# Kernel tuning notes

Hardware: AMD Instinct MI355X
Metric: run time of the kernel (lower is better)

The kernel has to match this reference:

```python
import jax, jax.numpy as jnp
import numpy as np

N, H, E, T, ED, AB = 50000, 64, 800000, 800000, 64, 16


def setup_inputs() -> dict:
    key = jax.random.key(0)
    ks = jax.random.split(key, 26)

    def nrm(k, shape, scale=1.0):
        return jax.random.normal(k, shape, dtype=jnp.float32) * scale

    d = {}
    d["s"] = nrm(ks[0], (N, H))
    d["v"] = nrm(ks[1], (N, H, 3))
    d["edge_index"] = jax.random.randint(ks[2], (2, E), 0, N, dtype=jnp.int32)
    d["edge_rbf"] = jax.random.uniform(ks[3], (E, ED), dtype=jnp.float32)
    raw_dir = jax.random.normal(ks[4], (E, 3), dtype=jnp.float32)
    d["edge_dir"] = raw_dir / jnp.linalg.norm(raw_dir, axis=-1, keepdims=True)
    d["triplet_kj"] = jax.random.randint(ks[5], (T,), 0, E, dtype=jnp.int32)
    d["triplet_ji"] = jax.random.randint(ks[6], (T,), 0, E, dtype=jnp.int32)
    d["angle_feat"] = jax.random.uniform(ks[7], (T, AB), dtype=jnp.float32)

    def lin(kw, kb, fan_in, fan_out):
        sc = 1.0 / np.sqrt(fan_in)
        return nrm(kw, (fan_in, fan_out), sc), nrm(kb, (fan_out,), sc)

    d["W_t1"], d["b_t1"] = lin(ks[8], ks[9], 2 * ED + AB, H)
    d["W_t2"], d["b_t2"] = lin(ks[10], ks[11], H, H)
    d["W_m1"], d["b_m1"] = lin(ks[12], ks[13], 2 * H + ED + H, H)
    d["W_m2"], d["b_m2"] = lin(ks[14], ks[15], H, 2 * H)
    d["W_u1"], d["b_u1"] = lin(ks[16], ks[17], 3 * H, H)
    d["W_u2"], d["b_u2"] = lin(ks[18], ks[19], H, H)
    d["W_g1"], d["b_g1"] = lin(ks[20], ks[21], 3 * H, H)
    d["W_g2"], d["b_g2"] = lin(ks[22], ks[23], H, H)
    d["ln_g"] = jnp.ones((H,), jnp.float32)
    d["ln_b"] = jnp.zeros((H,), jnp.float32)
    return d


def _mlp(x, W1, b1, W2, b2):
    return jax.nn.silu(x @ W1 + b1) @ W2 + b2


def reference(s, v, edge_index, edge_rbf, edge_dir, triplet_kj, triplet_ji,
              angle_feat, W_t1, b_t1, W_t2, b_t2, W_m1, b_m1, W_m2, b_m2,
              W_u1, b_u1, W_u2, b_u2, W_g1, b_g1, W_g2, b_g2, ln_g, ln_b):
    n_nodes, hid = s.shape
    n_edges = edge_rbf.shape[0]

    # 3-body triplet messages: gather two edge rbf rows + angle feature
    t_in = jnp.concatenate([edge_rbf[triplet_kj], edge_rbf[triplet_ji], angle_feat], axis=-1)
    t_msg = _mlp(t_in, W_t1, b_t1, W_t2, b_t2)                 # [T, H]
    angle_agg = jax.ops.segment_sum(t_msg, triplet_ji, num_segments=n_edges)  # [E, H]

    src, dst = edge_index[0], edge_index[1]
    msg_in = jnp.concatenate([s[src], s[dst], edge_rbf, angle_agg], axis=-1)  # [E, 4H]
    msg = _mlp(msg_in, W_m1, b_m1, W_m2, b_m2)                 # [E, 2H]
    m_s, m_v_coeff = jnp.split(msg, 2, axis=-1)

    agg_s = jax.ops.segment_sum(m_s, dst, num_segments=n_nodes)  # [N, H]
    m_v = m_v_coeff[:, :, None] * edge_dir[:, None, :]          # [E, H, 3]
    agg_v = jax.ops.segment_sum(m_v.reshape(n_edges, hid * 3), dst,
                                num_segments=n_nodes).reshape(n_nodes, hid, 3)

    v_norm = jnp.linalg.norm(v, axis=-1)                        # [N, H]
    ctx = jnp.concatenate([s, agg_s, v_norm], axis=-1)          # [N, 3H]
    s_new = s + _mlp(ctx, W_u1, b_u1, W_u2, b_u2)
    gate = jax.nn.sigmoid(_mlp(ctx, W_g1, b_g1, W_g2, b_g2))
    v_new = v + gate[..., None] * agg_v

    mu = s_new.mean(axis=-1, keepdims=True)
    var = s_new.var(axis=-1, keepdims=True)
    s_ln = (s_new - mu) / jnp.sqrt(var + 1e-5) * ln_g + ln_b
    s_out = jax.nn.silu(s_ln)
    return (s_out, v_new)
```

## Files before the change

kernel.cpp:

```cpp
#include <hip/hip_runtime.h>
#include <cstdint>
#include <cstddef>

#define NN 50000
#define NE 800000
#define NT 800000

typedef unsigned short u16;
typedef unsigned int u32;
typedef __attribute__((ext_vector_type(8))) short short8;
typedef __attribute__((ext_vector_type(4))) float f32x4;

__device__ __forceinline__ float silu_f(float x) { return x / (1.f + __expf(-x)); }
__device__ __forceinline__ float sigm_f(float x) { return 1.f / (1.f + __expf(-x)); }
__device__ __forceinline__ u16 f2b(float x) {
  u32 u = __float_as_uint(x);
  u32 r = u + 0x7fffu + ((u >> 16) & 1u);
  return (u16)(r >> 16);
}
__device__ __forceinline__ float b2f(u16 h) { return __uint_as_float(((u32)h) << 16); }

template <int RW>
__device__ __forceinline__ int lx(int r, int c) {
  return r * RW + ((((c >> 3) ^ (r & 7)) << 3) | (c & 7));
}

__global__ __launch_bounds__(256) void kcvt(const float* __restrict__ in,
                                            u16* __restrict__ out, int n4) {
  int i = blockIdx.x * 256 + threadIdx.x;
  if (i >= n4) return;
  float4 v = ((const float4*)in)[i];
  uint2 p;
  p.x = (u32)f2b(v.x) | ((u32)f2b(v.y) << 16);
  p.y = (u32)f2b(v.z) | ((u32)f2b(v.w) << 16);
  ((uint2*)out)[i] = p;
}

__global__ __launch_bounds__(256) void khist(const int* __restrict__ keys, int n,
                                             int* __restrict__ cnt) {
  int i = blockIdx.x * 256 + threadIdx.x;
  if (i < n) atomicAdd(&cnt[keys[i]], 1);
}

__global__ __launch_bounds__(256) void kscan1(const int* __restrict__ in, int n,
                                              int* __restrict__ out, int* __restrict__ bsum) {
  __shared__ int sh[256];
  int tid = threadIdx.x;
  size_t base = (size_t)blockIdx.x * 1024;
  int v[4];
  int acc = 0;
#pragma unroll
  for (int q = 0; q < 4; ++q) {
    size_t i = base + (size_t)tid * 4 + q;
    int x = (i < (size_t)n) ? in[i] : 0;
    v[q] = acc;
    acc += x;
  }
  sh[tid] = acc;
  __syncthreads();
  for (int off = 1; off < 256; off <<= 1) {
    int y = (tid >= off) ? sh[tid - off] : 0;
    __syncthreads();
    sh[tid] += y;
    __syncthreads();
  }
  int excl = (tid == 0) ? 0 : sh[tid - 1];
  if (tid == 255) bsum[blockIdx.x] = sh[255];
#pragma unroll
  for (int q = 0; q < 4; ++q) {
    size_t i = base + (size_t)tid * 4 + q;
    if (i < (size_t)n) out[i] = excl + v[q];
  }
}

__global__ __launch_bounds__(1024) void kscan2(int* __restrict__ bsum, int nb) {
  __shared__ int sh[1024];
  int tid = threadIdx.x;
  sh[tid] = (tid < nb) ? bsum[tid] : 0;
  __syncthreads();
  for (int off = 1; off < 1024; off <<= 1) {
    int y = (tid >= off) ? sh[tid - off] : 0;
    __syncthreads();
    sh[tid] += y;
    __syncthreads();
  }
  if (tid < nb) bsum[tid] = (tid == 0) ? 0 : sh[tid - 1];
}

__global__ __launch_bounds__(256) void kscan3(int* __restrict__ out, const int* __restrict__ bsum,
                                              int n, int total) {
  int i = blockIdx.x * 256 + threadIdx.x;
  if (i < n) out[i] += bsum[i >> 10];
  else if (i == n) out[n] = total;
}

__global__ __launch_bounds__(256) void kscatter_inv(const int* __restrict__ keys,
                                                    const int* __restrict__ off, int n,
                                                    int* __restrict__ cnt, int* __restrict__ inv) {
  int i = blockIdx.x * 256 + threadIdx.x;
  if (i < n) {
    int k = keys[i];
    int slot = off[k] + (atomicSub(&cnt[k], 1) - 1);
    inv[i] = slot;
  }
}

__global__ __launch_bounds__(256) void kscatter_inv_dir(const int* __restrict__ keys,
                                                        const int* __restrict__ off, int n,
                                                        int* __restrict__ cnt, int* __restrict__ inv,
                                                        const float* __restrict__ dir,
                                                        float* __restrict__ dir_s) {
  int i = blockIdx.x * 256 + threadIdx.x;
  if (i < n) {
    int k = keys[i];
    int slot = off[k] + (atomicSub(&cnt[k], 1) - 1);
    inv[i] = slot;
    dir_s[(size_t)slot * 3 + 0] = dir[(size_t)i * 3 + 0];
    dir_s[(size_t)slot * 3 + 1] = dir[(size_t)i * 3 + 1];
    dir_s[(size_t)slot * 3 + 2] = dir[(size_t)i * 3 + 2];
  }
}

__global__ __launch_bounds__(256) void kprepw(const float* __restrict__ W, int K, int Kp, int N,
                                              u16* __restrict__ out) {
  int tid = blockIdx.x * 256 + threadIdx.x;
  int total = (Kp / 32) * (N / 16) * 64;
  if (tid >= total) return;
  int l = tid & 63;
  int f = tid >> 6;
  int nt = f % (N / 16);
  int kt = f / (N / 16);
  int k0 = kt * 32 + (l >> 4) * 8;
  int n = nt * 16 + (l & 15);
  u16 vals[8];
#pragma unroll
  for (int j = 0; j < 8; ++j) {
    int kk = k0 + j;
    vals[j] = (kk < K) ? f2b(W[(size_t)kk * N + n]) : (u16)0;
  }
  uint4* dst = (uint4*)(out + (size_t)f * 512 + l * 8);
  uint4 p;
  p.x = (u32)vals[0] | ((u32)vals[1] << 16);
  p.y = (u32)vals[2] | ((u32)vals[3] << 16);
  p.z = (u32)vals[4] | ((u32)vals[5] << 16);
  p.w = (u32)vals[6] | ((u32)vals[7] << 16);
  *dst = p;
}

__global__ __launch_bounds__(256) void ktrip_mfma(
    const int* __restrict__ tkj, const int* __restrict__ tji,
    const u16* __restrict__ erbf_bf, const u16* __restrict__ afeat_bf,
    const int* __restrict__ tslot,
    const u16* __restrict__ Wp1, const float* __restrict__ b1,
    const u16* __restrict__ Wp2, const float* __restrict__ b2,
    u16* __restrict__ tmsg_s) {
  __shared__ u16 Xs[64 * 192];
  __shared__ u16 Hs[64 * 64];
  const int tid = threadIdx.x;
  const int l = tid & 63;
  const int w = tid >> 6;
  const int t0 = blockIdx.x * 64;

#pragma unroll
  for (int it = 0; it < 4; ++it) {
    int idx = it * 256 + tid;
    int sel = idx >> 9, r = (idx >> 3) & 63, ch = idx & 7;
    int t = t0 + r;
    int node = sel ? tji[t] : tkj[t];
    uint4 vv = *(const uint4*)&erbf_bf[(size_t)node * 64 + ch * 8];
    *(uint4*)&Xs[lx<192>(r, sel * 64 + ch * 8)] = vv;
  }
  {
    int r = tid >> 2, c = (tid & 3) * 4;
    uint2 p2 = *(const uint2*)&afeat_bf[(size_t)(t0 + r) * 16 + c];
    *(uint2*)&Xs[lx<192>(r, 128 + c)] = p2;
  }
#pragma unroll
  for (int i = 0; i < 2; ++i) {
    int idx = i * 256 + tid;
    int r = idx >> 3, c = 144 + (idx & 7) * 2;
    *(u32*)&Xs[lx<192>(r, c)] = 0;
  }
  __syncthreads();

  f32x4 acc1[4];
  {
    float bias = b1[w * 16 + (l & 15)];
#pragma unroll
    for (int mt = 0; mt < 4; ++mt) acc1[mt] = (f32x4){bias, bias, bias, bias};
    for (int ks = 0; ks < 5; ++ks) {
      short8 bf = *(const short8*)(Wp1 + ((size_t)(ks * 4 + w) * 64 + l) * 8);
#pragma unroll
      for (int mt = 0; mt < 4; ++mt) {
        short8 af = *(const short8*)&Xs[lx<192>(mt * 16 + (l & 15), ks * 32 + ((l >> 4) << 3))];
        acc1[mt] = __builtin_amdgcn_mfma_f32_16x16x32_bf16(af, bf, acc1[mt], 0, 0, 0);
      }
    }
  }
#pragma unroll
  for (int mt = 0; mt < 4; ++mt)
#pragma unroll
    for (int q = 0; q < 4; ++q) {
      int r = mt * 16 + (l >> 4) * 4 + q;
      Hs[lx<64>(r, w * 16 + (l & 15))] = f2b(silu_f(acc1[mt][q]));
    }
  __syncthreads();

  f32x4 acc2[4];
  {
    float bias = b2[w * 16 + (l & 15)];
#pragma unroll
    for (int mt = 0; mt < 4; ++mt) acc2[mt] = (f32x4){bias, bias, bias, bias};
    for (int ks = 0; ks < 2; ++ks) {
      short8 bf = *(const short8*)(Wp2 + ((size_t)(ks * 4 + w) * 64 + l) * 8);
#pragma unroll
      for (int mt = 0; mt < 4; ++mt) {
        short8 af = *(const short8*)&Hs[lx<64>(mt * 16 + (l & 15), ks * 32 + ((l >> 4) << 3))];
        acc2[mt] = __builtin_amdgcn_mfma_f32_16x16x32_bf16(af, bf, acc2[mt], 0, 0, 0);
      }
    }
  }
  __syncthreads();
#pragma unroll
  for (int mt = 0; mt < 4; ++mt)
#pragma unroll
    for (int q = 0; q < 4; ++q) {
      int r = mt * 16 + (l >> 4) * 4 + q;
      Xs[lx<64>(r, w * 16 + (l & 15))] = f2b(acc2[mt][q]);
    }
  __syncthreads();
  for (int i = 0; i < 2; ++i) {
    int idx = i * 256 + tid;
    int r = idx >> 3, c0 = (idx & 7) << 3;
    int slot = tslot[t0 + r];
    uint4 val = *(const uint4*)&Xs[lx<64>(r, c0)];
    *(uint4*)(tmsg_s + (size_t)slot * 64 + c0) = val;
  }
}

__global__ __launch_bounds__(256) void kmsg_mfma(
    const int* __restrict__ eidx, const u16* __restrict__ s_bf,
    const u16* __restrict__ erbf_bf,
    const int* __restrict__ toff, const u16* __restrict__ tmsg_s,
    const int* __restrict__ eslot,
    const u16* __restrict__ Wp1, const float* __restrict__ b1,
    const u16* __restrict__ Wp2, const float* __restrict__ b2,
    u16* __restrict__ msg_s) {
  __shared__ u16 Xs[64 * 256];
  __shared__ u16 Hs[64 * 64];
  const int tid = threadIdx.x;
  const int l = tid & 63;
  const int w = tid >> 6;
  const int e0 = blockIdx.x * 64;

#pragma unroll
  for (int i = 0; i < 2; ++i) {
    int idx = i * 256 + tid;
    int r = idx >> 3, c0 = (idx & 7) << 3;
    uint4 vv = *(const uint4*)&erbf_bf[(size_t)(e0 + r) * 64 + c0];
    *(uint4*)&Xs[lx<256>(r, 128 + c0)] = vv;
  }
#pragma unroll
  for (int it = 0; it < 4; ++it) {
    int idx = it * 256 + tid;
    int sel = idx >> 9, r = (idx >> 3) & 63, ch = idx & 7;
    int node = eidx[sel * NE + e0 + r];
    uint4 vv = *(const uint4*)&s_bf[(size_t)node * 64 + ch * 8];
    *(uint4*)&Xs[lx<256>(r, sel * 64 + ch * 8)] = vv;
  }
#pragma unroll
  for (int it = 0; it < 2; ++it) {
    int idx = it * 256 + tid;
    int r = idx >> 3, ch = idx & 7;
    int e = e0 + r;
    int r0 = toff[e], r1 = toff[e + 1];
    float a[8];
#pragma unroll
    for (int j = 0; j < 8; ++j) a[j] = 0.f;
    for (int ri = r0; ri < r1; ++ri) {
      uint4 pk = *(const uint4*)&tmsg_s[(size_t)ri * 64 + ch * 8];
      a[0] += b2f((u16)(pk.x & 0xffff)); a[1] += b2f((u16)(pk.x >> 16));
      a[2] += b2f((u16)(pk.y & 0xffff)); a[3] += b2f((u16)(pk.y >> 16));
      a[4] += b2f((u16)(pk.z & 0xffff)); a[5] += b2f((u16)(pk.z >> 16));
      a[6] += b2f((u16)(pk.w & 0xffff)); a[7] += b2f((u16)(pk.w >> 16));
    }
    uint4 p;
    p.x = (u32)f2b(a[0]) | ((u32)f2b(a[1]) << 16);
    p.y = (u32)f2b(a[2]) | ((u32)f2b(a[3]) << 16);
    p.z = (u32)f2b(a[4]) | ((u32)f2b(a[5]) << 16);
    p.w = (u32)f2b(a[6]) | ((u32)f2b(a[7]) << 16);
    *(uint4*)&Xs[lx<256>(r, 192 + ch * 8)] = p;
  }
  __syncthreads();

  f32x4 acc1[4];
  {
    float bias = b1[w * 16 + (l & 15)];
#pragma unroll
    for (int mt = 0; mt < 4; ++mt) acc1[mt] = (f32x4){bias, bias, bias, bias};
    for (int ks = 0; ks < 8; ++ks) {
      short8 bf = *(const short8*)(Wp1 + ((size_t)(ks * 4 + w) * 64 + l) * 8);
#pragma unroll
      for (int mt = 0; mt < 4; ++mt) {
        short8 af = *(const short8*)&Xs[lx<256>(mt * 16 + (l & 15), ks * 32 + ((l >> 4) << 3))];
        acc1[mt] = __builtin_amdgcn_mfma_f32_16x16x32_bf16(af, bf, acc1[mt], 0, 0, 0);
      }
    }
  }
#pragma unroll
  for (int mt = 0; mt < 4; ++mt)
#pragma unroll
    for (int q = 0; q < 4; ++q) {
      int r = mt * 16 + (l >> 4) * 4 + q;
      Hs[lx<64>(r, w * 16 + (l & 15))] = f2b(silu_f(acc1[mt][q]));
    }
  __syncthreads();

  f32x4 acc2[2][4];
#pragma unroll
  for (int pp = 0; pp < 2; ++pp) {
    int nt = w * 2 + pp;
    float bias = b2[nt * 16 + (l & 15)];
#pragma unroll
    for (int mt = 0; mt < 4; ++mt) acc2[pp][mt] = (f32x4){bias, bias, bias, bias};
    for (int ks = 0; ks < 2; ++ks) {
      short8 bf = *(const short8*)(Wp2 + ((size_t)(ks * 8 + nt) * 64 + l) * 8);
#pragma unroll
      for (int mt = 0; mt < 4; ++mt) {
        short8 af = *(const short8*)&Hs[lx<64>(mt * 16 + (l & 15), ks * 32 + ((l >> 4) << 3))];
        acc2[pp][mt] = __builtin_amdgcn_mfma_f32_16x16x32_bf16(af, bf, acc2[pp][mt], 0, 0, 0);
      }
    }
  }
  __syncthreads();
#pragma unroll
  for (int pp = 0; pp < 2; ++pp)
#pragma unroll
    for (int mt = 0; mt < 4; ++mt)
#pragma unroll
      for (int q = 0; q < 4; ++q) {
        int r = mt * 16 + (l >> 4) * 4 + q;
        Xs[lx<128>(r, (w * 2 + pp) * 16 + (l & 15))] = f2b(acc2[pp][mt][q]);
      }
  __syncthreads();
  for (int i = 0; i < 4; ++i) {
    int idx = i * 256 + tid;
    int r = idx >> 4, c0 = (idx & 15) << 3;
    int slot = eslot[e0 + r];
    uint4 val = *(const uint4*)&Xs[lx<128>(r, c0)];
    *(uint4*)(msg_s + (size_t)slot * 128 + c0) = val;
  }
}

__global__ __launch_bounds__(256) void kagg(
    const int* __restrict__ noff, const u16* __restrict__ msg_s,
    const float* __restrict__ dir_s,
    u16* __restrict__ aggs_bf, float* __restrict__ aggv) {
  const int lane = threadIdx.x & 63;
  const int wv = threadIdx.x >> 6;
  const int n = blockIdx.x * 4 + wv;
  if (n >= NN) return;
  const int r0 = noff[n], r1 = noff[n + 1];
  const int half = lane >> 5, m = lane & 31;
  float a0 = 0.f, a1 = 0.f;
  float v00 = 0.f, v01 = 0.f, v02 = 0.f, v10 = 0.f, v11 = 0.f, v12 = 0.f;
  for (int r = r0; r < r1; ++r) {
    u32 pk = *(const u32*)&msg_s[(size_t)r * 128 + lane * 2];
    float x0 = b2f((u16)(pk & 0xffff));
    float x1 = b2f((u16)(pk >> 16));
    if (half == 0) {
      a0 += x0; a1 += x1;
    } else {
      float dx = dir_s[(size_t)r * 3 + 0];
      float dy = dir_s[(size_t)r * 3 + 1];
      float dz = dir_s[(size_t)r * 3 + 2];
      v00 += x0 * dx; v01 += x0 * dy; v02 += x0 * dz;
      v10 += x1 * dx; v11 += x1 * dy; v12 += x1 * dz;
    }
  }
  if (half == 0) {
    *(u32*)&aggs_bf[(size_t)n * 64 + m * 2] = (u32)f2b(a0) | ((u32)f2b(a1) << 16);
  } else {
    float* av = aggv + (size_t)n * 192 + (size_t)(m * 2) * 3;
    av[0] = v00; av[1] = v01; av[2] = v02;
    av[3] = v10; av[4] = v11; av[5] = v12;
  }
}

__global__ __launch_bounds__(256) void knode_mfma(
    const u16* __restrict__ s_bf, const float* __restrict__ v,
    const u16* __restrict__ aggs_bf, const float* __restrict__ aggv,
    const u16* __restrict__ WpU1, const float* __restrict__ bU1,
    const u16* __restrict__ WpU2, const float* __restrict__ bU2,
    const u16* __restrict__ WpG1, const float* __restrict__ bG1,
    const u16* __restrict__ WpG2, const float* __restrict__ bG2,
    const float* __restrict__ lng, const float* __restrict__ lnb,
    float* __restrict__ outs, float* __restrict__ outv) {
  __shared__ __align__(16) char smem[64 * 192 * 2 + 2 * 64 * 64 * 2];
  u16* Xs = (u16*)smem;
  u16* Hu = (u16*)(smem + 64 * 192 * 2);
  u16* Hg = Hu + 64 * 64;
  float* Fs = (float*)smem;

  const int tid = threadIdx.x;
  const int l = tid & 63;
  const int w = tid >> 6;
  const int n0 = blockIdx.x * 64;

  for (int i = 0; i < 2; ++i) {
    int idx = i * 256 + tid;
    int r = idx >> 3, c0 = (idx & 7) << 3;
    int nr = n0 + r; if (nr >= NN) nr = NN - 1;
    uint4 a = *(const uint4*)&s_bf[(size_t)nr * 64 + c0];
    *(uint4*)&Xs[lx<192>(r, c0)] = a;
    uint4 b = *(const uint4*)&aggs_bf[(size_t)nr * 64 + c0];
    *(uint4*)&Xs[lx<192>(r, 64 + c0)] = b;
  }
  for (int it = 0; it < 16; ++it) {
    int idx = it * 256 + tid;
    int r = idx >> 6, c = idx & 63;
    int nr = n0 + r; if (nr >= NN) nr = NN - 1;
    const float* vp = v + (size_t)nr * 192 + c * 3;
    float x = vp[0], y = vp[1], z = vp[2];
    Xs[lx<192>(r, 128 + c)] = f2b(sqrtf(x * x + y * y + z * z));
  }
  __syncthreads();

  f32x4 au[4], ag[4];
  {
    float biu = bU1[w * 16 + (l & 15)], big = bG1[w * 16 + (l & 15)];
#pragma unroll
    for (int mt = 0; mt < 4; ++mt) {
      au[mt] = (f32x4){biu, biu, biu, biu};
      ag[mt] = (f32x4){big, big, big, big};
    }
    for (int ks = 0; ks < 6; ++ks) {
      short8 bu = *(const short8*)(WpU1 + ((size_t)(ks * 4 + w) * 64 + l) * 8);
      short8 bg = *(const short8*)(WpG1 + ((size_t)(ks * 4 + w) * 64 + l) * 8);
#pragma unroll
      for (int mt = 0; mt < 4; ++mt) {
        short8 af = *(const short8*)&Xs[lx<192>(mt * 16 + (l & 15), ks * 32 + ((l >> 4) << 3))];
        au[mt] = __builtin_amdgcn_mfma_f32_16x16x32_bf16(af, bu, au[mt], 0, 0, 0);
        ag[mt] = __builtin_amdgcn_mfma_f32_16x16x32_bf16(af, bg, ag[mt], 0, 0, 0);
      }
    }
  }
#pragma unroll
  for (int mt = 0; mt < 4; ++mt)
#pragma unroll
    for (int q = 0; q < 4; ++q) {
      int r = mt * 16 + (l >> 4) * 4 + q;
      Hu[lx<64>(r, w * 16 + (l & 15))] = f2b(silu_f(au[mt][q]));
      Hg[lx<64>(r, w * 16 + (l & 15))] = f2b(silu_f(ag[mt][q]));
    }
  __syncthreads();

  f32x4 ou[4], og[4];
  {
    float biu = bU2[w * 16 + (l & 15)], big = bG2[w * 16 + (l & 15)];
#pragma unroll
    for (int mt = 0; mt < 4; ++mt) {
      ou[mt] = (f32x4){biu, biu, biu, biu};
      og[mt] = (f32x4){big, big, big, big};
    }
    for (int ks = 0; ks < 2; ++ks) {
      short8 bu = *(const short8*)(WpU2 + ((size_t)(ks * 4 + w) * 64 + l) * 8);
      short8 bg = *(const short8*)(WpG2 + ((size_t)(ks * 4 + w) * 64 + l) * 8);
#pragma unroll
      for (int mt = 0; mt < 4; ++mt) {
        short8 afu = *(const short8*)&Hu[lx<64>(mt * 16 + (l & 15), ks * 32 + ((l >> 4) << 3))];
        ou[mt] = __builtin_amdgcn_mfma_f32_16x16x32_bf16(afu, bu, ou[mt], 0, 0, 0);
        short8 afg = *(const short8*)&Hg[lx<64>(mt * 16 + (l & 15), ks * 32 + ((l >> 4) << 3))];
        og[mt] = __builtin_amdgcn_mfma_f32_16x16x32_bf16(afg, bg, og[mt], 0, 0, 0);
      }
    }
  }
#pragma unroll
  for (int mt = 0; mt < 4; ++mt)
#pragma unroll
    for (int q = 0; q < 4; ++q) {
      int r = mt * 16 + (l >> 4) * 4 + q;
      ou[mt][q] += b2f(Xs[lx<192>(r, w * 16 + (l & 15))]);
    }
  __syncthreads();

#pragma unroll
  for (int mt = 0; mt < 4; ++mt)
#pragma unroll
    for (int q = 0; q < 4; ++q) {
      int r = mt * 16 + (l >> 4) * 4 + q;
      Fs[r * 68 + w * 16 + (l & 15)] = ou[mt][q];
    }
  __syncthreads();
  {
    int r = tid >> 2, c0 = (tid & 3) * 16;
    float xv[16];
#pragma unroll
    for (int j4 = 0; j4 < 4; ++j4) {
      float4 t = *(const float4*)&Fs[r * 68 + c0 + j4 * 4];
      xv[j4 * 4 + 0] = t.x; xv[j4 * 4 + 1] = t.y;
      xv[j4 * 4 + 2] = t.z; xv[j4 * 4 + 3] = t.w;
    }
    float sm = 0.f, sq = 0.f;
#pragma unroll
    for (int j = 0; j < 16; ++j) { sm += xv[j]; sq += xv[j] * xv[j]; }
    sm += __shfl_xor(sm, 1); sq += __shfl_xor(sq, 1);
    sm += __shfl_xor(sm, 2); sq += __shfl_xor(sq, 2);
    float mu = sm * (1.f / 64.f);
    float var = sq * (1.f / 64.f) - mu * mu;
    float rstd = rsqrtf(var + 1e-5f);
    if (n0 + r < NN) {
      float* op = outs + (size_t)(n0 + r) * 64 + c0;
#pragma unroll
      for (int j4 = 0; j4 < 4; ++j4) {
        float4 o;
        float y0 = (xv[j4 * 4 + 0] - mu) * rstd * lng[c0 + j4 * 4 + 0] + lnb[c0 + j4 * 4 + 0];
        float y1 = (xv[j4 * 4 + 1] - mu) * rstd * lng[c0 + j4 * 4 + 1] + lnb[c0 + j4 * 4 + 1];
        float y2 = (xv[j4 * 4 + 2] - mu) * rstd * lng[c0 + j4 * 4 + 2] + lnb[c0 + j4 * 4 + 2];
        float y3 = (xv[j4 * 4 + 3] - mu) * rstd * lng[c0 + j4 * 4 + 3] + lnb[c0 + j4 * 4 + 3];
        o.x = silu_f(y0); o.y = silu_f(y1); o.z = silu_f(y2); o.w = silu_f(y3);
        *(float4*)(op + j4 * 4) = o;
      }
    }
  }
  __syncthreads();

#pragma unroll
  for (int mt = 0; mt < 4; ++mt)
#pragma unroll
    for (int q = 0; q < 4; ++q) {
      int r = mt * 16 + (l >> 4) * 4 + q;
      Fs[r * 68 + w * 16 + (l & 15)] = og[mt][q];
    }
  __syncthreads();
  {
    int r = tid >> 2, c0 = (tid & 3) * 16;
    int nr = n0 + r;
    if (nr < NN) {
      float gate[16];
#pragma unroll
      for (int j = 0; j < 16; ++j) gate[j] = sigm_f(Fs[r * 68 + c0 + j]);
      const float4* vp = (const float4*)(v + (size_t)nr * 192 + c0 * 3);
      const float4* ap = (const float4*)(aggv + (size_t)nr * 192 + c0 * 3);
      float4* op = (float4*)(outv + (size_t)nr * 192 + c0 * 3);
#pragma unroll
      for (int j4 = 0; j4 < 12; ++j4) {
        float4 vv = vp[j4], av = ap[j4], o;
        o.x = vv.x + gate[(j4 * 4 + 0) / 3] * av.x;
        o.y = vv.y + gate[(j4 * 4 + 1) / 3] * av.y;
        o.z = vv.z + gate[(j4 * 4 + 2) / 3] * av.z;
        o.w = vv.w + gate[(j4 * 4 + 3) / 3] * av.w;
        op[j4] = o;
      }
    }
  }
}

extern "C" void kernel_launch(void* const* d_in, const int* in_sizes, int n_in,
                              void* d_out, int out_size, void* d_ws, size_t ws_size,
                              hipStream_t stream) {
  const float* s     = (const float*)d_in[0];
  const float* v     = (const float*)d_in[1];
  const int*   eidx  = (const int*)d_in[2];
  const float* erbf  = (const float*)d_in[3];
  const float* edir  = (const float*)d_in[4];
  const int*   tkj   = (const int*)d_in[5];
  const int*   tji   = (const int*)d_in[6];
  const float* afeat = (const float*)d_in[7];
  const float* W_t1  = (const float*)d_in[8];
  const float* b_t1  = (const float*)d_in[9];
  const float* W_t2  = (const float*)d_in[10];
  const float* b_t2  = (const float*)d_in[11];
  const float* W_m1  = (const float*)d_in[12];
  const float* b_m1  = (const float*)d_in[13];
  const float* W_m2  = (const float*)d_in[14];
  const float* b_m2  = (const float*)d_in[15];
  const float* W_u1  = (const float*)d_in[16];
  const float* b_u1  = (const float*)d_in[17];
  const float* W_u2  = (const float*)d_in[18];
  const float* b_u2  = (const float*)d_in[19];
  const float* W_g1  = (const float*)d_in[20];
  const float* b_g1  = (const float*)d_in[21];
  const float* W_g2  = (const float*)d_in[22];
  const float* b_g2  = (const float*)d_in[23];
  const float* ln_g  = (const float*)d_in[24];
  const float* ln_b  = (const float*)d_in[25];

  char* w = (char*)d_ws;
  auto alloc = [&](size_t bytes) -> char* {
    char* p = w;
    w += (bytes + 255) & ~(size_t)255;
    return p;
  };
  int* toff  = (int*)alloc((size_t)(NE + 1) * 4);
  int* noff  = (int*)alloc((size_t)(NN + 1) * 4);
  int* tcnt  = (int*)alloc((size_t)NE * 4);
  int* ncnt  = (int*)alloc((size_t)NN * 4);
  int* tslot = (int*)alloc((size_t)NT * 4);
  int* eslot = (int*)alloc((size_t)NE * 4);
  int* bsum  = (int*)alloc(1024 * 4);
  float* dir_s = (float*)alloc((size_t)NE * 3 * 4);
  u16* msg_s  = (u16*)alloc((size_t)NE * 128 * 2);
  u16* tmsg_s = (u16*)alloc((size_t)NT * 64 * 2);
  u16* erbf_bf = (u16*)alloc((size_t)NE * 64 * 2);
  u16* s_bf    = (u16*)alloc((size_t)NN * 64 * 2);
  u16* Wp_t1 = (u16*)alloc((size_t)5 * 4 * 512 * 2);
  u16* Wp_t2 = (u16*)alloc((size_t)2 * 4 * 512 * 2);
  u16* Wp_m1 = (u16*)alloc((size_t)8 * 4 * 512 * 2);
  u16* Wp_m2 = (u16*)alloc((size_t)2 * 8 * 512 * 2);
  u16* Wp_u1 = (u16*)alloc((size_t)6 * 4 * 512 * 2);
  u16* Wp_u2 = (u16*)alloc((size_t)2 * 4 * 512 * 2);
  u16* Wp_g1 = (u16*)alloc((size_t)6 * 4 * 512 * 2);
  u16* Wp_g2 = (u16*)alloc((size_t)2 * 4 * 512 * 2);
  u16* afeat_bf = msg_s;
  float* aggv = (float*)tmsg_s;
  u16* aggs_bf = tmsg_s + (size_t)NN * 384;

  hipMemsetAsync(tcnt, 0, (size_t)NE * 4, stream);
  hipMemsetAsync(ncnt, 0, (size_t)NN * 4, stream);

  kcvt<<<(NE * 16 + 255) / 256, 256, 0, stream>>>(erbf, erbf_bf, NE * 16);
  kcvt<<<(NN * 16 + 255) / 256, 256, 0, stream>>>(s, s_bf, NN * 16);
  kcvt<<<(NT * 4 + 255) / 256, 256, 0, stream>>>(afeat, afeat_bf, NT * 4);

  khist<<<(NT + 255) / 256, 256, 0, stream>>>(tji, NT, tcnt);
  khist<<<(NE + 255) / 256, 256, 0, stream>>>(eidx + NE, NE, ncnt);

  kscan1<<<(NE + 1023) / 1024, 256, 0, stream>>>(tcnt, NE, toff, bsum);
  kscan2<<<1, 1024, 0, stream>>>(bsum, (NE + 1023) / 1024);
  kscan3<<<(NE + 1 + 255) / 256, 256, 0, stream>>>(toff, bsum, NE, NT);
  kscatter_inv<<<(NT + 255) / 256, 256, 0, stream>>>(tji, toff, NT, tcnt, tslot);

  kscan1<<<(NN + 1023) / 1024, 256, 0, stream>>>(ncnt, NN, noff, bsum);
  kscan2<<<1, 1024, 0, stream>>>(bsum, (NN + 1023) / 1024);
  kscan3<<<(NN + 1 + 255) / 256, 256, 0, stream>>>(noff, bsum, NN, NE);
  kscatter_inv_dir<<<(NE + 255) / 256, 256, 0, stream>>>(eidx + NE, noff, NE, ncnt, eslot,
                                                         edir, dir_s);

  kprepw<<<5, 256, 0, stream>>>(W_t1, 144, 160, 64, Wp_t1);
  kprepw<<<2, 256, 0, stream>>>(W_t2, 64, 64, 64, Wp_t2);
  kprepw<<<8, 256, 0, stream>>>(W_m1, 256, 256, 64, Wp_m1);
  kprepw<<<4, 256, 0, stream>>>(W_m2, 64, 64, 128, Wp_m2);
  kprepw<<<6, 256, 0, stream>>>(W_u1, 192, 192, 64, Wp_u1);
  kprepw<<<2, 256, 0, stream>>>(W_u2, 64, 64, 64, Wp_u2);
  kprepw<<<6, 256, 0, stream>>>(W_g1, 192, 192, 64, Wp_g1);
  kprepw<<<2, 256, 0, stream>>>(W_g2, 64, 64, 64, Wp_g2);

  ktrip_mfma<<<NT / 64, 256, 0, stream>>>(tkj, tji, erbf_bf, afeat_bf, tslot,
                                          Wp_t1, b_t1, Wp_t2, b_t2, tmsg_s);
  kmsg_mfma<<<NE / 64, 256, 0, stream>>>(eidx, s_bf, erbf_bf, toff, tmsg_s, eslot,
                                         Wp_m1, b_m1, Wp_m2, b_m2, msg_s);
  kagg<<<(NN + 3) / 4, 256, 0, stream>>>(noff, msg_s, dir_s, aggs_bf, aggv);

  float* out_s = (float*)d_out;
  float* out_v = out_s + (size_t)NN * 64;
  knode_mfma<<<(NN + 63) / 64, 256, 0, stream>>>(s_bf, v, aggs_bf, aggv,
                                                 Wp_u1, b_u1, Wp_u2, b_u2,
                                                 Wp_g1, b_g1, Wp_g2, b_g2,
                                                 ln_g, ln_b, out_s, out_v);
}
```

Baseline: 726.7 us.

## Process triplets in sorted order, fuse afeat conversion into scatter, vectorize aggregation

The triplet kernel now iterates over triplets in their sorted-by-ji order, using an inverse permutation (tids), so its output rows are written contiguously instead of scattered through tslot. The angle-feature bf16 conversion is folded into the scatter kernel, which writes afeat already permuted into sorted order, removing one conversion launch. The node aggregation kernel is rewritten so each lane loads 16-byte chunks and four edge rows are processed per iteration, followed by a cross-lane shuffle reduction and vectorized stores. Trade-offs: the triplet kernel now does an extra indirect lookup per row, and the scatter kernel writes afeat at random slots.

```diff
diff --git a/kernel.cpp b/kernel.cpp
--- a/kernel.cpp
+++ b/kernel.cpp
@@ -94,14 +94,25 @@
   else if (i == n) out[n] = total;
 }
 
-__global__ __launch_bounds__(256) void kscatter_inv(const int* __restrict__ keys,
-                                                    const int* __restrict__ off, int n,
-                                                    int* __restrict__ cnt, int* __restrict__ inv) {
+__global__ __launch_bounds__(256) void kscatter_inv_afeat(
+    const int* __restrict__ keys, const int* __restrict__ off, int n,
+    int* __restrict__ cnt, int* __restrict__ tids,
+    const float* __restrict__ afeat, u16* __restrict__ afeat_s) {
   int i = blockIdx.x * 256 + threadIdx.x;
   if (i < n) {
     int k = keys[i];
     int slot = off[k] + (atomicSub(&cnt[k], 1) - 1);
-    inv[i] = slot;
+    tids[slot] = i;
+    const float4* src = (const float4*)(afeat + (size_t)i * 16);
+    uint2* dst = (uint2*)(afeat_s + (size_t)slot * 16);
+#pragma unroll
+    for (int q = 0; q < 4; ++q) {
+      float4 v = src[q];
+      uint2 p;
+      p.x = (u32)f2b(v.x) | ((u32)f2b(v.y) << 16);
+      p.y = (u32)f2b(v.z) | ((u32)f2b(v.w) << 16);
+      dst[q] = p;
+    }
   }
 }
 
@@ -149,8 +160,8 @@
 
 __global__ __launch_bounds__(256) void ktrip_mfma(
     const int* __restrict__ tkj, const int* __restrict__ tji,
-    const u16* __restrict__ erbf_bf, const u16* __restrict__ afeat_bf,
-    const int* __restrict__ tslot,
+    const u16* __restrict__ erbf_bf, const u16* __restrict__ afeat_s,
+    const int* __restrict__ tids,
     const u16* __restrict__ Wp1, const float* __restrict__ b1,
     const u16* __restrict__ Wp2, const float* __restrict__ b2,
     u16* __restrict__ tmsg_s) {
@@ -159,20 +170,20 @@
   const int tid = threadIdx.x;
   const int l = tid & 63;
   const int w = tid >> 6;
-  const int t0 = blockIdx.x * 64;
+  const int st0 = blockIdx.x * 64;
 
 #pragma unroll
   for (int it = 0; it < 4; ++it) {
     int idx = it * 256 + tid;
     int sel = idx >> 9, r = (idx >> 3) & 63, ch = idx & 7;
-    int t = t0 + r;
+    int t = tids[st0 + r];
     int node = sel ? tji[t] : tkj[t];
     uint4 vv = *(const uint4*)&erbf_bf[(size_t)node * 64 + ch * 8];
     *(uint4*)&Xs[lx<192>(r, sel * 64 + ch * 8)] = vv;
   }
   {
     int r = tid >> 2, c = (tid & 3) * 4;
-    uint2 p2 = *(const uint2*)&afeat_bf[(size_t)(t0 + r) * 16 + c];
+    uint2 p2 = *(const uint2*)&afeat_s[(size_t)(st0 + r) * 16 + c];
     *(uint2*)&Xs[lx<192>(r, 128 + c)] = p2;
   }
 #pragma unroll
@@ -232,9 +243,8 @@
   for (int i = 0; i < 2; ++i) {
     int idx = i * 256 + tid;
     int r = idx >> 3, c0 = (idx & 7) << 3;
-    int slot = tslot[t0 + r];
     uint4 val = *(const uint4*)&Xs[lx<64>(r, c0)];
-    *(uint4*)(tmsg_s + (size_t)slot * 64 + c0) = val;
+    *(uint4*)(tmsg_s + (size_t)(st0 + r) * 64 + c0) = val;
   }
 }
 
@@ -361,29 +371,64 @@
   const int n = blockIdx.x * 4 + wv;
   if (n >= NN) return;
   const int r0 = noff[n], r1 = noff[n + 1];
-  const int half = lane >> 5, m = lane & 31;
-  float a0 = 0.f, a1 = 0.f;
-  float v00 = 0.f, v01 = 0.f, v02 = 0.f, v10 = 0.f, v11 = 0.f, v12 = 0.f;
-  for (int r = r0; r < r1; ++r) {
-    u32 pk = *(const u32*)&msg_s[(size_t)r * 128 + lane * 2];
-    float x0 = b2f((u16)(pk & 0xffff));
-    float x1 = b2f((u16)(pk >> 16));
-    if (half == 0) {
-      a0 += x0; a1 += x1;
+  const int lrow = lane >> 4, lcol = lane & 15;
+  const bool is_ms = (lcol < 8);
+
+  float a[8];
+  float v0[8], v1[8], v2[8];
+#pragma unroll
+  for (int j = 0; j < 8; ++j) { a[j] = 0.f; v0[j] = 0.f; v1[j] = 0.f; v2[j] = 0.f; }
+
+  for (int r4 = r0; r4 < r1; r4 += 4) {
+    int r = r4 + lrow;
+    if (r < r1) {
+      uint4 pk = *(const uint4*)&msg_s[(size_t)r * 128 + lcol * 8];
+      float x[8];
+      x[0] = b2f((u16)(pk.x & 0xffff)); x[1] = b2f((u16)(pk.x >> 16));
+      x[2] = b2f((u16)(pk.y & 0xffff)); x[3] = b2f((u16)(pk.y >> 16));
+      x[4] = b2f((u16)(pk.z & 0xffff)); x[5] = b2f((u16)(pk.z >> 16));
+      x[6] = b2f((u16)(pk.w & 0xffff)); x[7] = b2f((u16)(pk.w >> 16));
+      if (is_ms) {
+#pragma unroll
+        for (int j = 0; j < 8; ++j) a[j] += x[j];
+      } else {
+        float dx = dir_s[(size_t)r * 3 + 0];
+        float dy = dir_s[(size_t)r * 3 + 1];
+        float dz = dir_s[(size_t)r * 3 + 2];
+#pragma unroll
+        for (int j = 0; j < 8; ++j) {
+          v0[j] += x[j] * dx; v1[j] += x[j] * dy; v2[j] += x[j] * dz;
+        }
+      }
+    }
+  }
+#pragma unroll
+  for (int j = 0; j < 8; ++j) {
+    a[j] += __shfl_xor(a[j], 16);  a[j] += __shfl_xor(a[j], 32);
+    v0[j] += __shfl_xor(v0[j], 16); v0[j] += __shfl_xor(v0[j], 32);
+    v1[j] += __shfl_xor(v1[j], 16); v1[j] += __shfl_xor(v1[j], 32);
+    v2[j] += __shfl_xor(v2[j], 16); v2[j] += __shfl_xor(v2[j], 32);
+  }
+  if (lrow == 0) {
+    if (is_ms) {
+      uint4 p;
+      p.x = (u32)f2b(a[0]) | ((u32)f2b(a[1]) << 16);
+      p.y = (u32)f2b(a[2]) | ((u32)f2b(a[3]) << 16);
+      p.z = (u32)f2b(a[4]) | ((u32)f2b(a[5]) << 16);
+      p.w = (u32)f2b(a[6]) | ((u32)f2b(a[7]) << 16);
+      *(uint4*)&aggs_bf[(size_t)n * 64 + lcol * 8] = p;
     } else {
-      float dx = dir_s[(size_t)r * 3 + 0];
-      float dy = dir_s[(size_t)r * 3 + 1];
-      float dz = dir_s[(size_t)r * 3 + 2];
-      v00 += x0 * dx; v01 += x0 * dy; v02 += x0 * dz;
-      v10 += x1 * dx; v11 += x1 * dy; v12 += x1 * dz;
-    }
-  }
-  if (half == 0) {
-    *(u32*)&aggs_bf[(size_t)n * 64 + m * 2] = (u32)f2b(a0) | ((u32)f2b(a1) << 16);
-  } else {
-    float* av = aggv + (size_t)n * 192 + (size_t)(m * 2) * 3;
-    av[0] = v00; av[1] = v01; av[2] = v02;
-    av[3] = v10; av[4] = v11; av[5] = v12;
+      int c0 = (lcol - 8) * 8;
+      float* av = aggv + (size_t)n * 192 + (size_t)c0 * 3;
+      float4 o0 = {v0[0], v1[0], v2[0], v0[1]};
+      float4 o1 = {v1[1], v2[1], v0[2], v1[2]};
+      float4 o2 = {v2[2], v0[3], v1[3], v2[3]};
+      float4 o3 = {v0[4], v1[4], v2[4], v0[5]};
+      float4 o4 = {v1[5], v2[5], v0[6], v1[6]};
+      float4 o5 = {v2[6], v0[7], v1[7], v2[7]};
+      float4* av4 = (float4*)av;
+      av4[0] = o0; av4[1] = o1; av4[2] = o2; av4[3] = o3; av4[4] = o4; av4[5] = o5;
+    }
   }
 }
 
@@ -596,7 +641,7 @@
   int* noff  = (int*)alloc((size_t)(NN + 1) * 4);
   int* tcnt  = (int*)alloc((size_t)NE * 4);
   int* ncnt  = (int*)alloc((size_t)NN * 4);
-  int* tslot = (int*)alloc((size_t)NT * 4);
+  int* tids  = (int*)alloc((size_t)NT * 4);
   int* eslot = (int*)alloc((size_t)NE * 4);
   int* bsum  = (int*)alloc(1024 * 4);
   float* dir_s = (float*)alloc((size_t)NE * 3 * 4);
@@ -612,7 +657,7 @@
   u16* Wp_u2 = (u16*)alloc((size_t)2 * 4 * 512 * 2);
   u16* Wp_g1 = (u16*)alloc((size_t)6 * 4 * 512 * 2);
   u16* Wp_g2 = (u16*)alloc((size_t)2 * 4 * 512 * 2);
-  u16* afeat_bf = msg_s;
+  u16* afeat_s = msg_s;
   float* aggv = (float*)tmsg_s;
   u16* aggs_bf = tmsg_s + (size_t)NN * 384;
 
@@ -621,7 +666,6 @@
 
   kcvt<<<(NE * 16 + 255) / 256, 256, 0, stream>>>(erbf, erbf_bf, NE * 16);
   kcvt<<<(NN * 16 + 255) / 256, 256, 0, stream>>>(s, s_bf, NN * 16);
-  kcvt<<<(NT * 4 + 255) / 256, 256, 0, stream>>>(afeat, afeat_bf, NT * 4);
 
   khist<<<(NT + 255) / 256, 256, 0, stream>>>(tji, NT, tcnt);
   khist<<<(NE + 255) / 256, 256, 0, stream>>>(eidx + NE, NE, ncnt);
@@ -629,7 +673,8 @@
   kscan1<<<(NE + 1023) / 1024, 256, 0, stream>>>(tcnt, NE, toff, bsum);
   kscan2<<<1, 1024, 0, stream>>>(bsum, (NE + 1023) / 1024);
   kscan3<<<(NE + 1 + 255) / 256, 256, 0, stream>>>(toff, bsum, NE, NT);
-  kscatter_inv<<<(NT + 255) / 256, 256, 0, stream>>>(tji, toff, NT, tcnt, tslot);
+  kscatter_inv_afeat<<<(NT + 255) / 256, 256, 0, stream>>>(tji, toff, NT, tcnt, tids,
+                                                           afeat, afeat_s);
 
   kscan1<<<(NN + 1023) / 1024, 256, 0, stream>>>(ncnt, NN, noff, bsum);
   kscan2<<<1, 1024, 0, stream>>>(bsum, (NN + 1023) / 1024);
@@ -646,7 +691,7 @@
   kprepw<<<6, 256, 0, stream>>>(W_g1, 192, 192, 64, Wp_g1);
   kprepw<<<2, 256, 0, stream>>>(W_g2, 64, 64, 64, Wp_g2);
 
-  ktrip_mfma<<<NT / 64, 256, 0, stream>>>(tkj, tji, erbf_bf, afeat_bf, tslot,
+  ktrip_mfma<<<NT / 64, 256, 0, stream>>>(tkj, tji, erbf_bf, afeat_s, tids,
                                           Wp_t1, b_t1, Wp_t2, b_t2, tmsg_s);
   kmsg_mfma<<<NE / 64, 256, 0, stream>>>(eidx, s_bf, erbf_bf, toff, tmsg_s, eslot,
                                          Wp_m1, b_m1, Wp_m2, b_m2, msg_s);
```

Measured after the change: 684.9 us. -5.8%, faster.
